# Kernel tuning notes

Measured on AMD Instinct MI355X. Metric: run time of the kernel, lower is better.

Reference implementation:

```python
import jax, jax.numpy as jnp
import numpy as np

BUCKET_SIZE = 64
LOOK_BACKWARD = 1
LOOK_FORWARD = 0  # causal => no look forward
CAUSAL = True


def look_around(x, backward, forward, pad_value):
    # x: [b, buckets, bucket_size, ...]; pads along the bucket axis and concats
    # shifted windows along the intra-bucket axis (dim=2), matching torch look_around.
    t = x.shape[1]
    pad_cfg = ((0, 0), (backward, forward)) + ((0, 0),) * (x.ndim - 2)
    padded = jnp.pad(x, pad_cfg, constant_values=pad_value)
    return jnp.concatenate([padded[:, i:i + t] for i in range(forward + backward + 1)], axis=2)


def setup_inputs() -> dict:
    key = jax.random.key(0)
    kq, kk, kv = jax.random.split(key, 3)
    shape = (4, 16, 4096, 64)  # [batch, heads, seq, head_dim]
    q = jax.random.normal(kq, shape, dtype=jnp.float32)
    k = jax.random.normal(kk, shape, dtype=jnp.float32)
    v = jax.random.normal(kv, shape, dtype=jnp.float32)
    return {"q": q, "k": k, "v": v}


def reference(q, k, v):
    shape = q.shape
    # merge batch and heads
    merge = lambda t: t.reshape(-1, t.shape[-2], t.shape[-1])
    q, k, v = merge(q), merge(k), merge(v)
    b, t, e = q.shape
    assert t % BUCKET_SIZE == 0
    buckets = t // BUCKET_SIZE

    ticker = jnp.arange(t, dtype=jnp.int32)[None, :]          # [1, t]
    b_t = ticker.reshape(1, buckets, BUCKET_SIZE)              # [1, buckets, bucket]

    bucket_fn = lambda x: x.reshape(b, buckets, BUCKET_SIZE, e)
    bq, bk, bv = bucket_fn(q), bucket_fn(k), bucket_fn(v)

    bk = look_around(bk, LOOK_BACKWARD, LOOK_FORWARD, 0.0)
    bv = look_around(bv, LOOK_BACKWARD, LOOK_FORWARD, 0.0)
    bq_t = b_t                                                 # query positions
    bq_k = look_around(b_t, LOOK_BACKWARD, LOOK_FORWARD, -1)   # key positions, -1 = pad

    scale = e ** (-0.5)
    dots = jnp.einsum('bnie,bnje->bnij', bq, bk) * scale
    mask_value = -jnp.finfo(dots.dtype).max

    if CAUSAL:
        causal_mask = bq_t[:, :, :, None] < bq_k[:, :, None, :]
        dots = jnp.where(causal_mask, mask_value, dots)

    pad_mask = bq_k[:, :, None, :] == -1
    dots = jnp.where(pad_mask, mask_value, dots)

    attn = jax.nn.softmax(dots, axis=-1)
    out = jnp.einsum('bnij,bnje->bnie', attn, bv)
    return out.reshape(shape)
```

## Files before the change

kernel.cpp:

```cpp
#include <hip/hip_runtime.h>
#include <hip/hip_bf16.h>

typedef __attribute__((ext_vector_type(8))) __bf16 bf16x8;
typedef __attribute__((ext_vector_type(4))) float f32x4;

#define SEQ   4096
#define HDIM  64
#define BKT   64

__device__ __forceinline__ unsigned f2bf_u(float f) {
    unsigned u = __float_as_uint(f);
    u += 0x7FFFu + ((u >> 16) & 1u);
    return u >> 16;
}
__device__ __forceinline__ unsigned pk2(float a, float b) {
    return f2bf_u(a) | (f2bf_u(b) << 16);
}
__device__ __forceinline__ int swzV(int row) {
    return ((row & 7) ^ ((row >> 3) & 7)) << 4;
}

__global__ void __launch_bounds__(256, 4) local_attn_kernel(
    const float* __restrict__ q, const float* __restrict__ k,
    const float* __restrict__ v, float* __restrict__ out)
{
    __shared__ __align__(16) unsigned short sK[128 * 64];
    __shared__ __align__(16) unsigned short sVt[64 * 128];

    const int tid = threadIdx.x;
    const int bid0 = blockIdx.x;
    const int lg = (bid0 & 7) * 512 + (bid0 >> 3);
    const int bh = lg >> 6;
    const int bucket = lg & 63;

    const int qoff = (bh * SEQ + bucket * BKT) * HDIM;
    const int koff = qoff - BKT * HDIM;

    const int lane = tid & 63;
    const int wid  = tid >> 6;
    const int g = lane >> 4, m = lane & 15;
    const int qbase = wid * 16;

    char* const sKb = reinterpret_cast<char*>(sK);
    char* const sVb = reinterpret_cast<char*>(sVt);

    float4 kreg[8], vreg[8], qreg[4];
    #pragma unroll
    for (int i = 0; i < 8; ++i) {
        const int flat = i * 1024 + tid * 4;
        kreg[i] = make_float4(0.f, 0.f, 0.f, 0.f);
        if (bucket > 0 || i >= 4)
            kreg[i] = *reinterpret_cast<const float4*>(k + koff + flat);
    }
    #pragma unroll
    for (int i = 0; i < 8; ++i) {
        const int kb = i * 16 + wid * 4;
        vreg[i] = make_float4(0.f, 0.f, 0.f, 0.f);
        if (bucket > 0 || i >= 4)
            vreg[i] = *reinterpret_cast<const float4*>(v + koff + (kb + g) * HDIM + m * 4);
    }
    #pragma unroll
    for (int h = 0; h < 2; ++h) {
        const float* qp = q + qoff + (qbase + m) * HDIM + h * 32 + g * 8;
        qreg[2 * h]     = *reinterpret_cast<const float4*>(qp);
        qreg[2 * h + 1] = *reinterpret_cast<const float4*>(qp + 4);
    }
    __builtin_amdgcn_sched_barrier(0);

    #pragma unroll
    for (int i = 0; i < 8; ++i) {
        const int flat = i * 1024 + tid * 4;
        const int row = flat >> 6, col = flat & 63;
        uint2 p;
        p.x = pk2(kreg[i].x, kreg[i].y);
        p.y = pk2(kreg[i].z, kreg[i].w);
        const int byte = (row * 128 + col * 2) ^ ((row & 7) << 4);
        *reinterpret_cast<uint2*>(sKb + byte) = p;
    }
    #pragma unroll
    for (int i = 0; i < 8; ++i) {
        const int kb = i * 16 + wid * 4;
        const int e0 = m * 4;
        const float4 f = vreg[i];
        const unsigned P0 = pk2(f.x, f.y);
        const unsigned P1 = pk2(f.z, f.w);
        const unsigned own  = (g < 2) ? P0 : P1;
        const unsigned send = (g < 2) ? P1 : P0;
        const unsigned R = __shfl_xor(send, 32);
        const unsigned T = __shfl_xor(own, 16);
        const unsigned U = __shfl_xor(R, 16);
        const unsigned A0 = (g < 2) ? own : R;
        const unsigned A1 = (g < 2) ? T : U;
        const unsigned A2 = (g < 2) ? R : own;
        const unsigned A3 = (g < 2) ? U : T;
        const int s = g & 1;
        const unsigned k0 = s ? A1 : A0, k1 = s ? A0 : A1;
        const unsigned k2 = s ? A3 : A2, k3 = s ? A2 : A3;
        const unsigned G0 = s ? ((k0 >> 16) | (k1 & 0xFFFF0000u)) : ((k0 & 0xFFFFu) | (k1 << 16));
        const unsigned G1 = s ? ((k2 >> 16) | (k3 & 0xFFFF0000u)) : ((k2 & 0xFFFFu) | (k3 << 16));
        const int er = e0 + g;
        const int byte = (er * 256 + kb * 2) ^ swzV(er);
        uint2 p; p.x = G0; p.y = G1;
        *reinterpret_cast<uint2*>(sVb + byte) = p;
    }
    const float scale = 0.125f * 1.44269504f;
    bf16x8 bq[2];
    #pragma unroll
    for (int h = 0; h < 2; ++h) {
        uint4 u;
        u.x = pk2(qreg[2 * h].x * scale, qreg[2 * h].y * scale);
        u.y = pk2(qreg[2 * h].z * scale, qreg[2 * h].w * scale);
        u.z = pk2(qreg[2 * h + 1].x * scale, qreg[2 * h + 1].y * scale);
        u.w = pk2(qreg[2 * h + 1].z * scale, qreg[2 * h + 1].w * scale);
        bq[h] = __builtin_bit_cast(bf16x8, u);
    }
    __syncthreads();

    f32x4 acc[8];
    #pragma unroll
    for (int c = 0; c < 8; ++c) acc[c] = (f32x4){0.f, 0.f, 0.f, 0.f};
    __builtin_amdgcn_s_setprio(1);
    #pragma unroll
    for (int c = 0; c < 8; ++c) {
        const int krow = c * 16 + m;
        #pragma unroll
        for (int h = 0; h < 2; ++h) {
            const int byte = (krow * 128 + h * 64 + g * 16) ^ ((m & 7) << 4);
            const bf16x8 ak = *reinterpret_cast<const bf16x8*>(sKb + byte);
            acc[c] = __builtin_amdgcn_mfma_f32_16x16x32_bf16(ak, bq[h], acc[c], 0, 0, 0);
        }
    }
    __builtin_amdgcn_s_setprio(0);

    const int qb = qbase + m;
    const int g4 = g * 4;
    float mx = -3e38f;
    #pragma unroll
    for (int c = 0; c < 8; ++c) {
        #pragma unroll
        for (int r = 0; r < 4; ++r) {
            const int kk = c * 16 + g4 + r;
            const bool dead = (c >= 4) ? (kk - 64 > qb) : (bucket == 0);
            const float s = dead ? -1e30f : acc[c][r];
            acc[c][r] = s;
            mx = fmaxf(mx, s);
        }
    }
    mx = fmaxf(mx, __shfl_xor(mx, 16));
    mx = fmaxf(mx, __shfl_xor(mx, 32));
    float sum = 0.f;
    uint2 pb[8];
    #pragma unroll
    for (int c = 0; c < 8; ++c) {
        const float p0 = __builtin_amdgcn_exp2f(acc[c][0] - mx);
        const float p1 = __builtin_amdgcn_exp2f(acc[c][1] - mx);
        const float p2 = __builtin_amdgcn_exp2f(acc[c][2] - mx);
        const float p3 = __builtin_amdgcn_exp2f(acc[c][3] - mx);
        sum += (p0 + p1) + (p2 + p3);
        pb[c].x = pk2(p0, p1);
        pb[c].y = pk2(p2, p3);
    }
    sum += __shfl_xor(sum, 16);
    sum += __shfl_xor(sum, 32);
    const float rl = 1.0f / sum;

    const int l0 = m + ((g & 1) << 5);
    const int l1 = l0 + 16;
    const bool hi = (g >> 1) != 0;
    bf16x8 bp[4];
    #pragma unroll
    for (int kt = 0; kt < 4; ++kt) {
        const unsigned a0x = __shfl(pb[2 * kt].x, l0),     a0y = __shfl(pb[2 * kt].y, l0);
        const unsigned a1x = __shfl(pb[2 * kt + 1].x, l0), a1y = __shfl(pb[2 * kt + 1].y, l0);
        const unsigned b0x = __shfl(pb[2 * kt].x, l1),     b0y = __shfl(pb[2 * kt].y, l1);
        const unsigned b1x = __shfl(pb[2 * kt + 1].x, l1), b1y = __shfl(pb[2 * kt + 1].y, l1);
        uint4 u;
        u.x = hi ? a1x : a0x;
        u.y = hi ? a1y : a0y;
        u.z = hi ? b1x : b0x;
        u.w = hi ? b1y : b0y;
        bp[kt] = __builtin_bit_cast(bf16x8, u);
    }

    f32x4 oacc[4];
    #pragma unroll
    for (int et = 0; et < 4; ++et) oacc[et] = (f32x4){0.f, 0.f, 0.f, 0.f};
    __builtin_amdgcn_s_setprio(1);
    #pragma unroll
    for (int et = 0; et < 4; ++et) {
        const int row = et * 16 + m;
        #pragma unroll
        for (int kt = 0; kt < 4; ++kt) {
            const int byte = (row * 256 + kt * 64 + g * 16) ^ swzV(row);
            const bf16x8 av = *reinterpret_cast<const bf16x8*>(sVb + byte);
            oacc[et] = __builtin_amdgcn_mfma_f32_16x16x32_bf16(av, bp[kt], oacc[et], 0, 0, 0);
        }
    }
    __builtin_amdgcn_s_setprio(0);

    const int qrow = qbase + m;
    #pragma unroll
    for (int et = 0; et < 4; ++et) {
        f32x4 o = oacc[et];
        o[0] *= rl; o[1] *= rl; o[2] *= rl; o[3] *= rl;
        *reinterpret_cast<float4*>(out + qoff + qrow * HDIM + et * 16 + g4) =
            *reinterpret_cast<float4*>(&o);
    }
}

extern "C" void kernel_launch(void* const* d_in, const int* in_sizes, int n_in,
                              void* d_out, int out_size, void* d_ws, size_t ws_size,
                              hipStream_t stream) {
    const float* q = (const float*)d_in[0];
    const float* k = (const float*)d_in[1];
    const float* v = (const float*)d_in[2];
    float* out = (float*)d_out;
    const int bh = in_sizes[0] / (SEQ * HDIM);
    const int nblocks = bh * (SEQ / BKT);
    hipLaunchKernelGGL(local_attn_kernel, dim3(nblocks), dim3(256), 0, stream,
                       q, k, v, out);
}
```

Measured before the change: 48.22 us.

## Process strips of four buckets per block with rotating K/V shared-memory slots

Each block now handles four consecutive buckets instead of one. K/V for the current bucket stay in shared memory and are reused as the look-back window for the next bucket. Loads for the next bucket are issued before the current bucket's compute, so they overlap. This removes the duplicate global reads of the previous bucket's K/V (roughly halving K/V traffic) and amortizes setup per block. In exchange the grid is 4x smaller (1024 blocks), launch bounds drop to 3 waves per SIMD, and two extra syncs per step serialize the strip.

```diff
diff --git a/kernel.cpp b/kernel.cpp
--- a/kernel.cpp
+++ b/kernel.cpp
@@ -4,9 +4,11 @@
 typedef __attribute__((ext_vector_type(8))) __bf16 bf16x8;
 typedef __attribute__((ext_vector_type(4))) float f32x4;
 
-#define SEQ   4096
-#define HDIM  64
-#define BKT   64
+#define SEQ    4096
+#define HDIM   64
+#define BKT    64
+#define STRIP  4
+#define KSLOTB 8192
 
 __device__ __forceinline__ unsigned f2bf_u(float f) {
     unsigned u = __float_as_uint(f);
@@ -20,191 +22,272 @@
     return ((row & 7) ^ ((row >> 3) & 7)) << 4;
 }
 
-__global__ void __launch_bounds__(256, 4) local_attn_kernel(
+__global__ void __launch_bounds__(256, 3) local_attn_kernel(
     const float* __restrict__ q, const float* __restrict__ k,
     const float* __restrict__ v, float* __restrict__ out)
 {
-    __shared__ __align__(16) unsigned short sK[128 * 64];
-    __shared__ __align__(16) unsigned short sVt[64 * 128];
+    __shared__ __align__(16) unsigned short sK[2 * 64 * 64];
+    __shared__ __align__(16) unsigned short sVt[2 * 64 * 64];
 
     const int tid = threadIdx.x;
-    const int bid0 = blockIdx.x;
-    const int lg = (bid0 & 7) * 512 + (bid0 >> 3);
-    const int bh = lg >> 6;
-    const int bucket = lg & 63;
-
-    const int qoff = (bh * SEQ + bucket * BKT) * HDIM;
-    const int koff = qoff - BKT * HDIM;
+    const int bid = blockIdx.x;
+    const int lg = (bid & 7) * 128 + (bid >> 3);
+    const int bh = lg >> 4;
+    const int strip = lg & 15;
+    const int b0 = strip * STRIP;
+
+    const int base = bh * SEQ * HDIM;
 
     const int lane = tid & 63;
     const int wid  = tid >> 6;
     const int g = lane >> 4, m = lane & 15;
+    const int g4 = g * 4;
     const int qbase = wid * 16;
+    const int qb = qbase + m;
 
     char* const sKb = reinterpret_cast<char*>(sK);
     char* const sVb = reinterpret_cast<char*>(sVt);
 
-    float4 kreg[8], vreg[8], qreg[4];
-    #pragma unroll
-    for (int i = 0; i < 8; ++i) {
-        const int flat = i * 1024 + tid * 4;
-        kreg[i] = make_float4(0.f, 0.f, 0.f, 0.f);
-        if (bucket > 0 || i >= 4)
-            kreg[i] = *reinterpret_cast<const float4*>(k + koff + flat);
-    }
-    #pragma unroll
-    for (int i = 0; i < 8; ++i) {
-        const int kb = i * 16 + wid * 4;
-        vreg[i] = make_float4(0.f, 0.f, 0.f, 0.f);
-        if (bucket > 0 || i >= 4)
-            vreg[i] = *reinterpret_cast<const float4*>(v + koff + (kb + g) * HDIM + m * 4);
-    }
-    #pragma unroll
-    for (int h = 0; h < 2; ++h) {
-        const float* qp = q + qoff + (qbase + m) * HDIM + h * 32 + g * 8;
-        qreg[2 * h]     = *reinterpret_cast<const float4*>(qp);
-        qreg[2 * h + 1] = *reinterpret_cast<const float4*>(qp + 4);
-    }
-    __builtin_amdgcn_sched_barrier(0);
-
-    #pragma unroll
-    for (int i = 0; i < 8; ++i) {
-        const int flat = i * 1024 + tid * 4;
-        const int row = flat >> 6, col = flat & 63;
-        uint2 p;
-        p.x = pk2(kreg[i].x, kreg[i].y);
-        p.y = pk2(kreg[i].z, kreg[i].w);
-        const int byte = (row * 128 + col * 2) ^ ((row & 7) << 4);
-        *reinterpret_cast<uint2*>(sKb + byte) = p;
-    }
-    #pragma unroll
-    for (int i = 0; i < 8; ++i) {
-        const int kb = i * 16 + wid * 4;
-        const int e0 = m * 4;
-        const float4 f = vreg[i];
-        const unsigned P0 = pk2(f.x, f.y);
-        const unsigned P1 = pk2(f.z, f.w);
-        const unsigned own  = (g < 2) ? P0 : P1;
-        const unsigned send = (g < 2) ? P1 : P0;
-        const unsigned R = __shfl_xor(send, 32);
-        const unsigned T = __shfl_xor(own, 16);
-        const unsigned U = __shfl_xor(R, 16);
-        const unsigned A0 = (g < 2) ? own : R;
-        const unsigned A1 = (g < 2) ? T : U;
-        const unsigned A2 = (g < 2) ? R : own;
-        const unsigned A3 = (g < 2) ? U : T;
-        const int s = g & 1;
-        const unsigned k0 = s ? A1 : A0, k1 = s ? A0 : A1;
-        const unsigned k2 = s ? A3 : A2, k3 = s ? A2 : A3;
-        const unsigned G0 = s ? ((k0 >> 16) | (k1 & 0xFFFF0000u)) : ((k0 & 0xFFFFu) | (k1 << 16));
-        const unsigned G1 = s ? ((k2 >> 16) | (k3 & 0xFFFF0000u)) : ((k2 & 0xFFFFu) | (k3 << 16));
-        const int er = e0 + g;
-        const int byte = (er * 256 + kb * 2) ^ swzV(er);
-        uint2 p; p.x = G0; p.y = G1;
-        *reinterpret_cast<uint2*>(sVb + byte) = p;
-    }
     const float scale = 0.125f * 1.44269504f;
     bf16x8 bq[2];
+
+    {
+        const int win0 = base + (b0 - 1) * BKT * HDIM;
+        float4 kreg[8], vreg[8], qreg[4];
+        #pragma unroll
+        for (int i = 0; i < 8; ++i) {
+            kreg[i] = make_float4(0.f, 0.f, 0.f, 0.f);
+            if (strip > 0 || i >= 4)
+                kreg[i] = *reinterpret_cast<const float4*>(k + win0 + i * 1024 + tid * 4);
+        }
+        #pragma unroll
+        for (int i = 0; i < 8; ++i) {
+            const int kb = i * 16 + wid * 4;
+            vreg[i] = make_float4(0.f, 0.f, 0.f, 0.f);
+            if (strip > 0 || i >= 4)
+                vreg[i] = *reinterpret_cast<const float4*>(v + win0 + (kb + g) * HDIM + m * 4);
+        }
+        const int qoff0 = base + b0 * BKT * HDIM;
+        #pragma unroll
+        for (int h = 0; h < 2; ++h) {
+            const float* qp = q + qoff0 + qb * HDIM + h * 32 + g * 8;
+            qreg[2 * h]     = *reinterpret_cast<const float4*>(qp);
+            qreg[2 * h + 1] = *reinterpret_cast<const float4*>(qp + 4);
+        }
+        __builtin_amdgcn_sched_barrier(0);
+        #pragma unroll
+        for (int i = 0; i < 8; ++i) {
+            const int flat = i * 1024 + tid * 4;
+            const int lr = (flat >> 6) & 63, col = flat & 63;
+            uint2 p;
+            p.x = pk2(kreg[i].x, kreg[i].y);
+            p.y = pk2(kreg[i].z, kreg[i].w);
+            const int byte = ((i < 4) ? KSLOTB : 0) + ((lr * 128 + col * 2) ^ ((lr & 7) << 4));
+            *reinterpret_cast<uint2*>(sKb + byte) = p;
+        }
+        #pragma unroll
+        for (int i = 0; i < 8; ++i) {
+            const int kbl = (i * 16 + wid * 4) & 63;
+            const float4 f = vreg[i];
+            const unsigned P0 = pk2(f.x, f.y);
+            const unsigned P1 = pk2(f.z, f.w);
+            const unsigned own  = (g < 2) ? P0 : P1;
+            const unsigned send = (g < 2) ? P1 : P0;
+            const unsigned R = __shfl_xor(send, 32);
+            const unsigned T = __shfl_xor(own, 16);
+            const unsigned U = __shfl_xor(R, 16);
+            const unsigned A0 = (g < 2) ? own : R;
+            const unsigned A1 = (g < 2) ? T : U;
+            const unsigned A2 = (g < 2) ? R : own;
+            const unsigned A3 = (g < 2) ? U : T;
+            const int sdx = g & 1;
+            const unsigned k0 = sdx ? A1 : A0, k1 = sdx ? A0 : A1;
+            const unsigned k2 = sdx ? A3 : A2, k3 = sdx ? A2 : A3;
+            const unsigned G0 = sdx ? ((k0 >> 16) | (k1 & 0xFFFF0000u)) : ((k0 & 0xFFFFu) | (k1 << 16));
+            const unsigned G1 = sdx ? ((k2 >> 16) | (k3 & 0xFFFF0000u)) : ((k2 & 0xFFFFu) | (k3 << 16));
+            const int er = m * 4 + g;
+            const int byte = ((i < 4) ? KSLOTB : 0) + ((er * 128 + kbl * 2) ^ swzV(er));
+            uint2 p; p.x = G0; p.y = G1;
+            *reinterpret_cast<uint2*>(sVb + byte) = p;
+        }
+        #pragma unroll
+        for (int h = 0; h < 2; ++h) {
+            uint4 u;
+            u.x = pk2(qreg[2 * h].x * scale, qreg[2 * h].y * scale);
+            u.y = pk2(qreg[2 * h].z * scale, qreg[2 * h].w * scale);
+            u.z = pk2(qreg[2 * h + 1].x * scale, qreg[2 * h + 1].y * scale);
+            u.w = pk2(qreg[2 * h + 1].z * scale, qreg[2 * h + 1].w * scale);
+            bq[h] = __builtin_bit_cast(bf16x8, u);
+        }
+        __syncthreads();
+    }
+
     #pragma unroll
-    for (int h = 0; h < 2; ++h) {
-        uint4 u;
-        u.x = pk2(qreg[2 * h].x * scale, qreg[2 * h].y * scale);
-        u.y = pk2(qreg[2 * h].z * scale, qreg[2 * h].w * scale);
-        u.z = pk2(qreg[2 * h + 1].x * scale, qreg[2 * h + 1].y * scale);
-        u.w = pk2(qreg[2 * h + 1].z * scale, qreg[2 * h + 1].w * scale);
-        bq[h] = __builtin_bit_cast(bf16x8, u);
-    }
-    __syncthreads();
-
-    f32x4 acc[8];
-    #pragma unroll
-    for (int c = 0; c < 8; ++c) acc[c] = (f32x4){0.f, 0.f, 0.f, 0.f};
-    __builtin_amdgcn_s_setprio(1);
-    #pragma unroll
-    for (int c = 0; c < 8; ++c) {
-        const int krow = c * 16 + m;
-        #pragma unroll
-        for (int h = 0; h < 2; ++h) {
-            const int byte = (krow * 128 + h * 64 + g * 16) ^ ((m & 7) << 4);
-            const bf16x8 ak = *reinterpret_cast<const bf16x8*>(sKb + byte);
-            acc[c] = __builtin_amdgcn_mfma_f32_16x16x32_bf16(ak, bq[h], acc[c], 0, 0, 0);
-        }
-    }
-    __builtin_amdgcn_s_setprio(0);
-
-    const int qb = qbase + m;
-    const int g4 = g * 4;
-    float mx = -3e38f;
-    #pragma unroll
-    for (int c = 0; c < 8; ++c) {
-        #pragma unroll
-        for (int r = 0; r < 4; ++r) {
-            const int kk = c * 16 + g4 + r;
-            const bool dead = (c >= 4) ? (kk - 64 > qb) : (bucket == 0);
-            const float s = dead ? -1e30f : acc[c][r];
-            acc[c][r] = s;
-            mx = fmaxf(mx, s);
-        }
-    }
-    mx = fmaxf(mx, __shfl_xor(mx, 16));
-    mx = fmaxf(mx, __shfl_xor(mx, 32));
-    float sum = 0.f;
-    uint2 pb[8];
-    #pragma unroll
-    for (int c = 0; c < 8; ++c) {
-        const float p0 = __builtin_amdgcn_exp2f(acc[c][0] - mx);
-        const float p1 = __builtin_amdgcn_exp2f(acc[c][1] - mx);
-        const float p2 = __builtin_amdgcn_exp2f(acc[c][2] - mx);
-        const float p3 = __builtin_amdgcn_exp2f(acc[c][3] - mx);
-        sum += (p0 + p1) + (p2 + p3);
-        pb[c].x = pk2(p0, p1);
-        pb[c].y = pk2(p2, p3);
-    }
-    sum += __shfl_xor(sum, 16);
-    sum += __shfl_xor(sum, 32);
-    const float rl = 1.0f / sum;
-
-    const int l0 = m + ((g & 1) << 5);
-    const int l1 = l0 + 16;
-    const bool hi = (g >> 1) != 0;
-    bf16x8 bp[4];
-    #pragma unroll
-    for (int kt = 0; kt < 4; ++kt) {
-        const unsigned a0x = __shfl(pb[2 * kt].x, l0),     a0y = __shfl(pb[2 * kt].y, l0);
-        const unsigned a1x = __shfl(pb[2 * kt + 1].x, l0), a1y = __shfl(pb[2 * kt + 1].y, l0);
-        const unsigned b0x = __shfl(pb[2 * kt].x, l1),     b0y = __shfl(pb[2 * kt].y, l1);
-        const unsigned b1x = __shfl(pb[2 * kt + 1].x, l1), b1y = __shfl(pb[2 * kt + 1].y, l1);
-        uint4 u;
-        u.x = hi ? a1x : a0x;
-        u.y = hi ? a1y : a0y;
-        u.z = hi ? b1x : b0x;
-        u.w = hi ? b1y : b0y;
-        bp[kt] = __builtin_bit_cast(bf16x8, u);
-    }
-
-    f32x4 oacc[4];
-    #pragma unroll
-    for (int et = 0; et < 4; ++et) oacc[et] = (f32x4){0.f, 0.f, 0.f, 0.f};
-    __builtin_amdgcn_s_setprio(1);
-    #pragma unroll
-    for (int et = 0; et < 4; ++et) {
-        const int row = et * 16 + m;
+    for (int jj = 0; jj < STRIP; ++jj) {
+        const int qoffj = base + (b0 + jj) * BKT * HDIM;
+        const int scur = (jj & 1) * KSLOTB;
+        const int spre = scur ^ KSLOTB;
+
+        float4 kn[4], vn[4], qn[4];
+        if (jj < STRIP - 1) {
+            const int noff = qoffj + BKT * HDIM;
+            #pragma unroll
+            for (int i = 0; i < 4; ++i)
+                kn[i] = *reinterpret_cast<const float4*>(k + noff + i * 1024 + tid * 4);
+            #pragma unroll
+            for (int i = 0; i < 4; ++i) {
+                const int kbl = i * 16 + wid * 4;
+                vn[i] = *reinterpret_cast<const float4*>(v + noff + (kbl + g) * HDIM + m * 4);
+            }
+            #pragma unroll
+            for (int h = 0; h < 2; ++h) {
+                const float* qp = q + noff + qb * HDIM + h * 32 + g * 8;
+                qn[2 * h]     = *reinterpret_cast<const float4*>(qp);
+                qn[2 * h + 1] = *reinterpret_cast<const float4*>(qp + 4);
+            }
+            __builtin_amdgcn_sched_barrier(0);
+        }
+
+        f32x4 acc[8];
+        #pragma unroll
+        for (int c = 0; c < 8; ++c) acc[c] = (f32x4){0.f, 0.f, 0.f, 0.f};
+        __builtin_amdgcn_s_setprio(1);
+        #pragma unroll
+        for (int c = 0; c < 8; ++c) {
+            const int lr = (c & 3) * 16 + m;
+            const int sb = (c < 4) ? spre : scur;
+            #pragma unroll
+            for (int h = 0; h < 2; ++h) {
+                const int byte = sb + ((lr * 128 + h * 64 + g * 16) ^ ((m & 7) << 4));
+                const bf16x8 ak = *reinterpret_cast<const bf16x8*>(sKb + byte);
+                acc[c] = __builtin_amdgcn_mfma_f32_16x16x32_bf16(ak, bq[h], acc[c], 0, 0, 0);
+            }
+        }
+        __builtin_amdgcn_s_setprio(0);
+
+        const bool dead_prev = (strip == 0 && jj == 0);
+        float mx = -3e38f;
+        #pragma unroll
+        for (int c = 0; c < 8; ++c) {
+            #pragma unroll
+            for (int r = 0; r < 4; ++r) {
+                const int kk = c * 16 + g4 + r;
+                const bool dead = (c >= 4) ? (kk - 64 > qb) : dead_prev;
+                const float s = dead ? -1e30f : acc[c][r];
+                acc[c][r] = s;
+                mx = fmaxf(mx, s);
+            }
+        }
+        mx = fmaxf(mx, __shfl_xor(mx, 16));
+        mx = fmaxf(mx, __shfl_xor(mx, 32));
+        float sum = 0.f;
+        uint2 pb[8];
+        #pragma unroll
+        for (int c = 0; c < 8; ++c) {
+            const float p0 = __builtin_amdgcn_exp2f(acc[c][0] - mx);
+            const float p1 = __builtin_amdgcn_exp2f(acc[c][1] - mx);
+            const float p2 = __builtin_amdgcn_exp2f(acc[c][2] - mx);
+            const float p3 = __builtin_amdgcn_exp2f(acc[c][3] - mx);
+            sum += (p0 + p1) + (p2 + p3);
+            pb[c].x = pk2(p0, p1);
+            pb[c].y = pk2(p2, p3);
+        }
+        sum += __shfl_xor(sum, 16);
+        sum += __shfl_xor(sum, 32);
+        const float rl = 1.0f / sum;
+
+        const int l0 = m + ((g & 1) << 5);
+        const int l1 = l0 + 16;
+        const bool hi = (g >> 1) != 0;
+        bf16x8 bp[4];
         #pragma unroll
         for (int kt = 0; kt < 4; ++kt) {
-            const int byte = (row * 256 + kt * 64 + g * 16) ^ swzV(row);
-            const bf16x8 av = *reinterpret_cast<const bf16x8*>(sVb + byte);
-            oacc[et] = __builtin_amdgcn_mfma_f32_16x16x32_bf16(av, bp[kt], oacc[et], 0, 0, 0);
-        }
-    }
-    __builtin_amdgcn_s_setprio(0);
-
-    const int qrow = qbase + m;
-    #pragma unroll
-    for (int et = 0; et < 4; ++et) {
-        f32x4 o = oacc[et];
-        o[0] *= rl; o[1] *= rl; o[2] *= rl; o[3] *= rl;
-        *reinterpret_cast<float4*>(out + qoff + qrow * HDIM + et * 16 + g4) =
-            *reinterpret_cast<float4*>(&o);
+            const unsigned a0x = __shfl(pb[2 * kt].x, l0),     a0y = __shfl(pb[2 * kt].y, l0);
+            const unsigned a1x = __shfl(pb[2 * kt + 1].x, l0), a1y = __shfl(pb[2 * kt + 1].y, l0);
+            const unsigned b0x = __shfl(pb[2 * kt].x, l1),     b0y = __shfl(pb[2 * kt].y, l1);
+            const unsigned b1x = __shfl(pb[2 * kt + 1].x, l1), b1y = __shfl(pb[2 * kt + 1].y, l1);
+            uint4 u;
+            u.x = hi ? a1x : a0x;
+            u.y = hi ? a1y : a0y;
+            u.z = hi ? b1x : b0x;
+            u.w = hi ? b1y : b0y;
+            bp[kt] = __builtin_bit_cast(bf16x8, u);
+        }
+
+        f32x4 oacc[4];
+        #pragma unroll
+        for (int et = 0; et < 4; ++et) oacc[et] = (f32x4){0.f, 0.f, 0.f, 0.f};
+        __builtin_amdgcn_s_setprio(1);
+        #pragma unroll
+        for (int et = 0; et < 4; ++et) {
+            const int row = et * 16 + m;
+            #pragma unroll
+            for (int kt = 0; kt < 4; ++kt) {
+                const int sb = (kt < 2) ? spre : scur;
+                const int kcol = (kt & 1) * 32 + g * 8;
+                const int byte = sb + ((row * 128 + kcol * 2) ^ swzV(row));
+                const bf16x8 av = *reinterpret_cast<const bf16x8*>(sVb + byte);
+                oacc[et] = __builtin_amdgcn_mfma_f32_16x16x32_bf16(av, bp[kt], oacc[et], 0, 0, 0);
+            }
+        }
+        __builtin_amdgcn_s_setprio(0);
+
+        #pragma unroll
+        for (int et = 0; et < 4; ++et) {
+            f32x4 o = oacc[et];
+            o[0] *= rl; o[1] *= rl; o[2] *= rl; o[3] *= rl;
+            *reinterpret_cast<float4*>(out + qoffj + qb * HDIM + et * 16 + g4) =
+                *reinterpret_cast<float4*>(&o);
+        }
+
+        if (jj < STRIP - 1) {
+            __syncthreads();
+            #pragma unroll
+            for (int i = 0; i < 4; ++i) {
+                const int flat = i * 1024 + tid * 4;
+                const int lr = flat >> 6, col = flat & 63;
+                uint2 p;
+                p.x = pk2(kn[i].x, kn[i].y);
+                p.y = pk2(kn[i].z, kn[i].w);
+                const int byte = spre + ((lr * 128 + col * 2) ^ ((lr & 7) << 4));
+                *reinterpret_cast<uint2*>(sKb + byte) = p;
+            }
+            #pragma unroll
+            for (int i = 0; i < 4; ++i) {
+                const int kbl = i * 16 + wid * 4;
+                const float4 f = vn[i];
+                const unsigned P0 = pk2(f.x, f.y);
+                const unsigned P1 = pk2(f.z, f.w);
+                const unsigned own  = (g < 2) ? P0 : P1;
+                const unsigned send = (g < 2) ? P1 : P0;
+                const unsigned R = __shfl_xor(send, 32);
+                const unsigned T = __shfl_xor(own, 16);
+                const unsigned U = __shfl_xor(R, 16);
+                const unsigned A0 = (g < 2) ? own : R;
+                const unsigned A1 = (g < 2) ? T : U;
+                const unsigned A2 = (g < 2) ? R : own;
+                const unsigned A3 = (g < 2) ? U : T;
+                const int sdx = g & 1;
+                const unsigned k0 = sdx ? A1 : A0, k1 = sdx ? A0 : A1;
+                const unsigned k2 = sdx ? A3 : A2, k3 = sdx ? A2 : A3;
+                const unsigned G0 = sdx ? ((k0 >> 16) | (k1 & 0xFFFF0000u)) : ((k0 & 0xFFFFu) | (k1 << 16));
+                const unsigned G1 = sdx ? ((k2 >> 16) | (k3 & 0xFFFF0000u)) : ((k2 & 0xFFFFu) | (k3 << 16));
+                const int er = m * 4 + g;
+                const int byte = spre + ((er * 128 + kbl * 2) ^ swzV(er));
+                uint2 p; p.x = G0; p.y = G1;
+                *reinterpret_cast<uint2*>(sVb + byte) = p;
+            }
+            #pragma unroll
+            for (int h = 0; h < 2; ++h) {
+                uint4 u;
+                u.x = pk2(qn[2 * h].x * scale, qn[2 * h].y * scale);
+                u.y = pk2(qn[2 * h].z * scale, qn[2 * h].w * scale);
+                u.z = pk2(qn[2 * h + 1].x * scale, qn[2 * h + 1].y * scale);
+                u.w = pk2(qn[2 * h + 1].z * scale, qn[2 * h + 1].w * scale);
+                bq[h] = __builtin_bit_cast(bf16x8, u);
+            }
+            __syncthreads();
+        }
     }
 }
 
@@ -216,7 +299,7 @@
     const float* v = (const float*)d_in[2];
     float* out = (float*)d_out;
     const int bh = in_sizes[0] / (SEQ * HDIM);
-    const int nblocks = bh * (SEQ / BKT);
+    const int nblocks = bh * (SEQ / BKT / STRIP);
     hipLaunchKernelGGL(local_attn_kernel, dim3(nblocks), dim3(256), 0, stream,
                        q, k, v, out);
 }
```

New measurement: 51.81 us. +7.4%, slower.

## Load K directly into LDS as fp32 via global_load_lds and convert at read

Applied to the files above, without the earlier changes.

K tiles are now copied straight from global memory into shared memory in fp32 with global_load_lds, with a pre-swizzled source address, instead of staging through registers and packing to bf16. Conversion to bf16 happens when the MFMA operands are read, using a cheap round-half-up perm-based packer. For bucket 0 the padded first half is loaded from a valid offset and still masked later. This removes the register staging and VGPR pressure for K but doubles LDS usage for K (32KB) and adds conversion work inside the QK loop, which may hurt occupancy.

```diff
diff --git a/kernel.cpp b/kernel.cpp
--- a/kernel.cpp
+++ b/kernel.cpp
@@ -16,6 +16,11 @@
 __device__ __forceinline__ unsigned pk2(float a, float b) {
     return f2bf_u(a) | (f2bf_u(b) << 16);
 }
+__device__ __forceinline__ unsigned pkhi(float a, float b) {
+    const unsigned ua = __float_as_uint(a) + 0x8000u;
+    const unsigned ub = __float_as_uint(b) + 0x8000u;
+    return __builtin_amdgcn_perm(ub, ua, 0x07060302u);
+}
 __device__ __forceinline__ int swzV(int row) {
     return ((row & 7) ^ ((row >> 3) & 7)) << 4;
 }
@@ -24,7 +29,7 @@
     const float* __restrict__ q, const float* __restrict__ k,
     const float* __restrict__ v, float* __restrict__ out)
 {
-    __shared__ __align__(16) unsigned short sK[128 * 64];
+    __shared__ __align__(16) float sK[128 * 64];
     __shared__ __align__(16) unsigned short sVt[64 * 128];
 
     const int tid = threadIdx.x;
@@ -39,19 +44,13 @@
     const int lane = tid & 63;
     const int wid  = tid >> 6;
     const int g = lane >> 4, m = lane & 15;
+    const int g4 = g * 4;
     const int qbase = wid * 16;
 
     char* const sKb = reinterpret_cast<char*>(sK);
     char* const sVb = reinterpret_cast<char*>(sVt);
 
-    float4 kreg[8], vreg[8], qreg[4];
-    #pragma unroll
-    for (int i = 0; i < 8; ++i) {
-        const int flat = i * 1024 + tid * 4;
-        kreg[i] = make_float4(0.f, 0.f, 0.f, 0.f);
-        if (bucket > 0 || i >= 4)
-            kreg[i] = *reinterpret_cast<const float4*>(k + koff + flat);
-    }
+    float4 vreg[8], qreg[4];
     #pragma unroll
     for (int i = 0; i < 8; ++i) {
         const int kb = i * 16 + wid * 4;
@@ -65,22 +64,27 @@
         qreg[2 * h]     = *reinterpret_cast<const float4*>(qp);
         qreg[2 * h + 1] = *reinterpret_cast<const float4*>(qp + 4);
     }
+
+    {
+        const int fix = (bucket == 0 && wid < 2) ? (BKT * HDIM) : 0;
+        #pragma unroll
+        for (int i = 0; i < 8; ++i) {
+            const int instr = wid * 8 + i;
+            const int A = instr * 1024 + lane * 16;
+            const int row = A >> 8;
+            const int colb = (A & 255) ^ ((row & 7) << 4);
+            const float* src = k + koff + fix + row * HDIM + (colb >> 2);
+            __builtin_amdgcn_global_load_lds(
+                (const __attribute__((address_space(1))) void*)src,
+                (__attribute__((address_space(3))) void*)(sKb + instr * 1024),
+                16, 0, 0);
+        }
+    }
     __builtin_amdgcn_sched_barrier(0);
 
-    #pragma unroll
-    for (int i = 0; i < 8; ++i) {
-        const int flat = i * 1024 + tid * 4;
-        const int row = flat >> 6, col = flat & 63;
-        uint2 p;
-        p.x = pk2(kreg[i].x, kreg[i].y);
-        p.y = pk2(kreg[i].z, kreg[i].w);
-        const int byte = (row * 128 + col * 2) ^ ((row & 7) << 4);
-        *reinterpret_cast<uint2*>(sKb + byte) = p;
-    }
     #pragma unroll
     for (int i = 0; i < 8; ++i) {
         const int kb = i * 16 + wid * 4;
-        const int e0 = m * 4;
         const float4 f = vreg[i];
         const unsigned P0 = pk2(f.x, f.y);
         const unsigned P1 = pk2(f.z, f.w);
@@ -93,12 +97,12 @@
         const unsigned A1 = (g < 2) ? T : U;
         const unsigned A2 = (g < 2) ? R : own;
         const unsigned A3 = (g < 2) ? U : T;
-        const int s = g & 1;
-        const unsigned k0 = s ? A1 : A0, k1 = s ? A0 : A1;
-        const unsigned k2 = s ? A3 : A2, k3 = s ? A2 : A3;
-        const unsigned G0 = s ? ((k0 >> 16) | (k1 & 0xFFFF0000u)) : ((k0 & 0xFFFFu) | (k1 << 16));
-        const unsigned G1 = s ? ((k2 >> 16) | (k3 & 0xFFFF0000u)) : ((k2 & 0xFFFFu) | (k3 << 16));
-        const int er = e0 + g;
+        const int sdx = g & 1;
+        const unsigned k0 = sdx ? A1 : A0, k1 = sdx ? A0 : A1;
+        const unsigned k2 = sdx ? A3 : A2, k3 = sdx ? A2 : A3;
+        const unsigned G0 = sdx ? ((k0 >> 16) | (k1 & 0xFFFF0000u)) : ((k0 & 0xFFFFu) | (k1 << 16));
+        const unsigned G1 = sdx ? ((k2 >> 16) | (k3 & 0xFFFF0000u)) : ((k2 & 0xFFFFu) | (k3 << 16));
+        const int er = m * 4 + g;
         const int byte = (er * 256 + kb * 2) ^ swzV(er);
         uint2 p; p.x = G0; p.y = G1;
         *reinterpret_cast<uint2*>(sVb + byte) = p;
@@ -122,18 +126,25 @@
     __builtin_amdgcn_s_setprio(1);
     #pragma unroll
     for (int c = 0; c < 8; ++c) {
-        const int krow = c * 16 + m;
+        const int rb = (c * 16 + m) * 256;
+        const int s = (m & 7) << 4;
         #pragma unroll
         for (int h = 0; h < 2; ++h) {
-            const int byte = (krow * 128 + h * 64 + g * 16) ^ ((m & 7) << 4);
-            const bf16x8 ak = *reinterpret_cast<const bf16x8*>(sKb + byte);
+            const int B = h * 128 + g * 32;
+            const f32x4 lo = *reinterpret_cast<const f32x4*>(sKb + rb + (B ^ s));
+            const f32x4 hi = *reinterpret_cast<const f32x4*>(sKb + rb + ((B + 16) ^ s));
+            uint4 u;
+            u.x = pkhi(lo[0], lo[1]);
+            u.y = pkhi(lo[2], lo[3]);
+            u.z = pkhi(hi[0], hi[1]);
+            u.w = pkhi(hi[2], hi[3]);
+            const bf16x8 ak = __builtin_bit_cast(bf16x8, u);
             acc[c] = __builtin_amdgcn_mfma_f32_16x16x32_bf16(ak, bq[h], acc[c], 0, 0, 0);
         }
     }
     __builtin_amdgcn_s_setprio(0);
 
     const int qb = qbase + m;
-    const int g4 = g * 4;
     float mx = -3e38f;
     #pragma unroll
     for (int c = 0; c < 8; ++c) {
@@ -166,7 +177,7 @@
 
     const int l0 = m + ((g & 1) << 5);
     const int l1 = l0 + 16;
-    const bool hi = (g >> 1) != 0;
+    const bool hi2 = (g >> 1) != 0;
     bf16x8 bp[4];
     #pragma unroll
     for (int kt = 0; kt < 4; ++kt) {
@@ -175,10 +186,10 @@
         const unsigned b0x = __shfl(pb[2 * kt].x, l1),     b0y = __shfl(pb[2 * kt].y, l1);
         const unsigned b1x = __shfl(pb[2 * kt + 1].x, l1), b1y = __shfl(pb[2 * kt + 1].y, l1);
         uint4 u;
-        u.x = hi ? a1x : a0x;
-        u.y = hi ? a1y : a0y;
-        u.z = hi ? b1x : b0x;
-        u.w = hi ? b1y : b0y;
+        u.x = hi2 ? a1x : a0x;
+        u.y = hi2 ? a1y : a0y;
+        u.z = hi2 ? b1x : b0x;
+        u.w = hi2 ? b1y : b0y;
         bp[kt] = __builtin_bit_cast(bf16x8, u);
     }
 
```

After: 52.28 us. 1.08x slower.

## Alias K and V shared buffers and defer V load to raise occupancy

Applied to the files above, without the earlier changes.

The kernel now uses one 16KB shared buffer for both K and the transposed V instead of two, with extra barriers so V overwrites K only after QK^T is done. V global loads move after the QK MFMA, so fewer registers are live at once. Launch bounds go from 4 to 8 blocks per CU so more blocks can fit. In exchange, the V load latency is now exposed after the first GEMM and there are two more block-wide syncs.

```diff
diff --git a/kernel.cpp b/kernel.cpp
--- a/kernel.cpp
+++ b/kernel.cpp
@@ -20,12 +20,11 @@
     return ((row & 7) ^ ((row >> 3) & 7)) << 4;
 }
 
-__global__ void __launch_bounds__(256, 4) local_attn_kernel(
+__global__ void __launch_bounds__(256, 8) local_attn_kernel(
     const float* __restrict__ q, const float* __restrict__ k,
     const float* __restrict__ v, float* __restrict__ out)
 {
-    __shared__ __align__(16) unsigned short sK[128 * 64];
-    __shared__ __align__(16) unsigned short sVt[64 * 128];
+    __shared__ __align__(16) unsigned short sBuf[128 * 64];
 
     const int tid = threadIdx.x;
     const int bid0 = blockIdx.x;
@@ -39,25 +38,18 @@
     const int lane = tid & 63;
     const int wid  = tid >> 6;
     const int g = lane >> 4, m = lane & 15;
+    const int g4 = g * 4;
     const int qbase = wid * 16;
 
-    char* const sKb = reinterpret_cast<char*>(sK);
-    char* const sVb = reinterpret_cast<char*>(sVt);
-
-    float4 kreg[8], vreg[8], qreg[4];
+    char* const sB = reinterpret_cast<char*>(sBuf);
+
+    float4 kreg[8], qreg[4];
     #pragma unroll
     for (int i = 0; i < 8; ++i) {
         const int flat = i * 1024 + tid * 4;
         kreg[i] = make_float4(0.f, 0.f, 0.f, 0.f);
         if (bucket > 0 || i >= 4)
             kreg[i] = *reinterpret_cast<const float4*>(k + koff + flat);
-    }
-    #pragma unroll
-    for (int i = 0; i < 8; ++i) {
-        const int kb = i * 16 + wid * 4;
-        vreg[i] = make_float4(0.f, 0.f, 0.f, 0.f);
-        if (bucket > 0 || i >= 4)
-            vreg[i] = *reinterpret_cast<const float4*>(v + koff + (kb + g) * HDIM + m * 4);
     }
     #pragma unroll
     for (int h = 0; h < 2; ++h) {
@@ -75,12 +67,83 @@
         p.x = pk2(kreg[i].x, kreg[i].y);
         p.y = pk2(kreg[i].z, kreg[i].w);
         const int byte = (row * 128 + col * 2) ^ ((row & 7) << 4);
-        *reinterpret_cast<uint2*>(sKb + byte) = p;
-    }
+        *reinterpret_cast<uint2*>(sB + byte) = p;
+    }
+    const float scale = 0.125f * 1.44269504f;
+    bf16x8 bq[2];
+    #pragma unroll
+    for (int h = 0; h < 2; ++h) {
+        uint4 u;
+        u.x = pk2(qreg[2 * h].x * scale, qreg[2 * h].y * scale);
+        u.y = pk2(qreg[2 * h].z * scale, qreg[2 * h].w * scale);
+        u.z = pk2(qreg[2 * h + 1].x * scale, qreg[2 * h + 1].y * scale);
+        u.w = pk2(qreg[2 * h + 1].z * scale, qreg[2 * h + 1].w * scale);
+        bq[h] = __builtin_bit_cast(bf16x8, u);
+    }
+    __syncthreads();
+
+    f32x4 acc[8];
+    #pragma unroll
+    for (int c = 0; c < 8; ++c) acc[c] = (f32x4){0.f, 0.f, 0.f, 0.f};
+    __builtin_amdgcn_s_setprio(1);
+    #pragma unroll
+    for (int c = 0; c < 8; ++c) {
+        const int krow = c * 16 + m;
+        #pragma unroll
+        for (int h = 0; h < 2; ++h) {
+            const int byte = (krow * 128 + h * 64 + g * 16) ^ ((m & 7) << 4);
+            const bf16x8 ak = *reinterpret_cast<const bf16x8*>(sB + byte);
+            acc[c] = __builtin_amdgcn_mfma_f32_16x16x32_bf16(ak, bq[h], acc[c], 0, 0, 0);
+        }
+    }
+    __builtin_amdgcn_s_setprio(0);
+
+    float4 vreg[8];
     #pragma unroll
     for (int i = 0; i < 8; ++i) {
         const int kb = i * 16 + wid * 4;
-        const int e0 = m * 4;
+        vreg[i] = make_float4(0.f, 0.f, 0.f, 0.f);
+        if (bucket > 0 || i >= 4)
+            vreg[i] = *reinterpret_cast<const float4*>(v + koff + (kb + g) * HDIM + m * 4);
+    }
+    __builtin_amdgcn_sched_barrier(0);
+
+    const int qb = qbase + m;
+    float mx = -3e38f;
+    #pragma unroll
+    for (int c = 0; c < 8; ++c) {
+        #pragma unroll
+        for (int r = 0; r < 4; ++r) {
+            const int kk = c * 16 + g4 + r;
+            const bool dead = (c >= 4) ? (kk - 64 > qb) : (bucket == 0);
+            const float s = dead ? -1e30f : acc[c][r];
+            acc[c][r] = s;
+            mx = fmaxf(mx, s);
+        }
+    }
+    mx = fmaxf(mx, __shfl_xor(mx, 16));
+    mx = fmaxf(mx, __shfl_xor(mx, 32));
+    float sum = 0.f;
+    uint2 pb[8];
+    #pragma unroll
+    for (int c = 0; c < 8; ++c) {
+        const float p0 = __builtin_amdgcn_exp2f(acc[c][0] - mx);
+        const float p1 = __builtin_amdgcn_exp2f(acc[c][1] - mx);
+        const float p2 = __builtin_amdgcn_exp2f(acc[c][2] - mx);
+        const float p3 = __builtin_amdgcn_exp2f(acc[c][3] - mx);
+        sum += (p0 + p1) + (p2 + p3);
+        pb[c].x = pk2(p0, p1);
+        pb[c].y = pk2(p2, p3);
+    }
+    sum += __shfl_xor(sum, 16);
+    sum += __shfl_xor(sum, 32);
+    const float rl = 1.0f / sum;
+
+    __syncthreads();
+
+    #pragma unroll
+    for (int i = 0; i < 8; ++i) {
+        const int kb = i * 16 + wid * 4;
         const float4 f = vreg[i];
         const unsigned P0 = pk2(f.x, f.y);
         const unsigned P1 = pk2(f.z, f.w);
@@ -93,80 +156,20 @@
         const unsigned A1 = (g < 2) ? T : U;
         const unsigned A2 = (g < 2) ? R : own;
         const unsigned A3 = (g < 2) ? U : T;
-        const int s = g & 1;
-        const unsigned k0 = s ? A1 : A0, k1 = s ? A0 : A1;
-        const unsigned k2 = s ? A3 : A2, k3 = s ? A2 : A3;
-        const unsigned G0 = s ? ((k0 >> 16) | (k1 & 0xFFFF0000u)) : ((k0 & 0xFFFFu) | (k1 << 16));
-        const unsigned G1 = s ? ((k2 >> 16) | (k3 & 0xFFFF0000u)) : ((k2 & 0xFFFFu) | (k3 << 16));
-        const int er = e0 + g;
+        const int sdx = g & 1;
+        const unsigned k0 = sdx ? A1 : A0, k1 = sdx ? A0 : A1;
+        const unsigned k2 = sdx ? A3 : A2, k3 = sdx ? A2 : A3;
+        const unsigned G0 = sdx ? ((k0 >> 16) | (k1 & 0xFFFF0000u)) : ((k0 & 0xFFFFu) | (k1 << 16));
+        const unsigned G1 = sdx ? ((k2 >> 16) | (k3 & 0xFFFF0000u)) : ((k2 & 0xFFFFu) | (k3 << 16));
+        const int er = m * 4 + g;
         const int byte = (er * 256 + kb * 2) ^ swzV(er);
         uint2 p; p.x = G0; p.y = G1;
-        *reinterpret_cast<uint2*>(sVb + byte) = p;
-    }
-    const float scale = 0.125f * 1.44269504f;
-    bf16x8 bq[2];
-    #pragma unroll
-    for (int h = 0; h < 2; ++h) {
-        uint4 u;
-        u.x = pk2(qreg[2 * h].x * scale, qreg[2 * h].y * scale);
-        u.y = pk2(qreg[2 * h].z * scale, qreg[2 * h].w * scale);
-        u.z = pk2(qreg[2 * h + 1].x * scale, qreg[2 * h + 1].y * scale);
-        u.w = pk2(qreg[2 * h + 1].z * scale, qreg[2 * h + 1].w * scale);
-        bq[h] = __builtin_bit_cast(bf16x8, u);
-    }
-    __syncthreads();
-
-    f32x4 acc[8];
-    #pragma unroll
-    for (int c = 0; c < 8; ++c) acc[c] = (f32x4){0.f, 0.f, 0.f, 0.f};
-    __builtin_amdgcn_s_setprio(1);
-    #pragma unroll
-    for (int c = 0; c < 8; ++c) {
-        const int krow = c * 16 + m;
-        #pragma unroll
-        for (int h = 0; h < 2; ++h) {
-            const int byte = (krow * 128 + h * 64 + g * 16) ^ ((m & 7) << 4);
-            const bf16x8 ak = *reinterpret_cast<const bf16x8*>(sKb + byte);
-            acc[c] = __builtin_amdgcn_mfma_f32_16x16x32_bf16(ak, bq[h], acc[c], 0, 0, 0);
-        }
-    }
-    __builtin_amdgcn_s_setprio(0);
-
-    const int qb = qbase + m;
-    const int g4 = g * 4;
-    float mx = -3e38f;
-    #pragma unroll
-    for (int c = 0; c < 8; ++c) {
-        #pragma unroll
-        for (int r = 0; r < 4; ++r) {
-            const int kk = c * 16 + g4 + r;
-            const bool dead = (c >= 4) ? (kk - 64 > qb) : (bucket == 0);
-            const float s = dead ? -1e30f : acc[c][r];
-            acc[c][r] = s;
-            mx = fmaxf(mx, s);
-        }
-    }
-    mx = fmaxf(mx, __shfl_xor(mx, 16));
-    mx = fmaxf(mx, __shfl_xor(mx, 32));
-    float sum = 0.f;
-    uint2 pb[8];
-    #pragma unroll
-    for (int c = 0; c < 8; ++c) {
-        const float p0 = __builtin_amdgcn_exp2f(acc[c][0] - mx);
-        const float p1 = __builtin_amdgcn_exp2f(acc[c][1] - mx);
-        const float p2 = __builtin_amdgcn_exp2f(acc[c][2] - mx);
-        const float p3 = __builtin_amdgcn_exp2f(acc[c][3] - mx);
-        sum += (p0 + p1) + (p2 + p3);
-        pb[c].x = pk2(p0, p1);
-        pb[c].y = pk2(p2, p3);
-    }
-    sum += __shfl_xor(sum, 16);
-    sum += __shfl_xor(sum, 32);
-    const float rl = 1.0f / sum;
+        *reinterpret_cast<uint2*>(sB + byte) = p;
+    }
 
     const int l0 = m + ((g & 1) << 5);
     const int l1 = l0 + 16;
-    const bool hi = (g >> 1) != 0;
+    const bool hi2 = (g >> 1) != 0;
     bf16x8 bp[4];
     #pragma unroll
     for (int kt = 0; kt < 4; ++kt) {
@@ -175,12 +178,13 @@
         const unsigned b0x = __shfl(pb[2 * kt].x, l1),     b0y = __shfl(pb[2 * kt].y, l1);
         const unsigned b1x = __shfl(pb[2 * kt + 1].x, l1), b1y = __shfl(pb[2 * kt + 1].y, l1);
         uint4 u;
-        u.x = hi ? a1x : a0x;
-        u.y = hi ? a1y : a0y;
-        u.z = hi ? b1x : b0x;
-        u.w = hi ? b1y : b0y;
+        u.x = hi2 ? a1x : a0x;
+        u.y = hi2 ? a1y : a0y;
+        u.z = hi2 ? b1x : b0x;
+        u.w = hi2 ? b1y : b0y;
         bp[kt] = __builtin_bit_cast(bf16x8, u);
     }
+    __syncthreads();
 
     f32x4 oacc[4];
     #pragma unroll
@@ -192,7 +196,7 @@
         #pragma unroll
         for (int kt = 0; kt < 4; ++kt) {
             const int byte = (row * 256 + kt * 64 + g * 16) ^ swzV(row);
-            const bf16x8 av = *reinterpret_cast<const bf16x8*>(sVb + byte);
+            const bf16x8 av = *reinterpret_cast<const bf16x8*>(sB + byte);
             oacc[et] = __builtin_amdgcn_mfma_f32_16x16x32_bf16(av, bp[kt], oacc[et], 0, 0, 0);
         }
     }
```

Result: slower. 110.1 us (+128.2%).
